# Kernel optimization log

Measured on AMD Instinct MI355X. Metric: run time of the kernel, lower is better.

Reference implementation:

```python
import jax, jax.numpy as jnp
import numpy as np

B, T, I, H = 64, 2048, 256, 256


def setup_inputs() -> dict:
    key = jax.random.key(0)
    ks = jax.random.split(key, 6)
    s = 1.0 / np.sqrt(H)
    x = jax.random.normal(ks[0], (B, T, I), dtype=jnp.float32)
    att_weights = jax.random.uniform(ks[1], (B, T), dtype=jnp.float32)
    lengths = jax.random.randint(ks[2], (B,), 1, T + 1, dtype=jnp.int32)
    W_ih = jax.random.uniform(ks[3], (3 * H, I), minval=-s, maxval=s, dtype=jnp.float32)
    W_hh = jax.random.uniform(ks[4], (3 * H, H), minval=-s, maxval=s, dtype=jnp.float32)
    b_ih = jax.random.uniform(ks[5], (3 * H,), minval=-s, maxval=s, dtype=jnp.float32)
    b_hh = jax.random.uniform(jax.random.fold_in(key, 7), (3 * H,), minval=-s, maxval=s, dtype=jnp.float32)
    return {"x": x, "att_weights": att_weights, "lengths": lengths,
            "W_ih": W_ih, "W_hh": W_hh, "b_ih": b_ih, "b_hh": b_hh}


def reference(x, att_weights, lengths, W_ih, W_hh, b_ih, b_hh):
    # x: [B, T, I]; att_weights: [B, T]; lengths: [B]
    Bv, Tv, _ = x.shape
    Hv = W_hh.shape[1]
    # Padded equivalent of the packed-sequence loop: update h only while t < length.
    mask = jnp.arange(Tv)[None, :] < lengths[:, None]  # [B, T]

    def step(h, inp):
        xt, wt, mt = inp  # [B, I], [B], [B]
        gi = xt @ W_ih.T + b_ih  # [B, 3H]
        gh = h @ W_hh.T + b_hh   # [B, 3H]
        i_r, i_z, i_n = jnp.split(gi, 3, axis=-1)
        h_r, h_z, h_n = jnp.split(gh, 3, axis=-1)
        r = jax.nn.sigmoid(i_r + h_r)
        z = jax.nn.sigmoid(i_z + h_z)
        n = jnp.tanh(i_n + r * h_n)
        h_new = (1.0 - z) * n + z * h  # GRUCell output
        w = wt[:, None]
        h_gated = w * h_new + (1.0 - w) * h  # attention gating
        h = jnp.where(mt[:, None], h_gated, h)
        return h, None

    h0 = jnp.zeros((Bv, Hv), dtype=x.dtype)
    xs = (jnp.swapaxes(x, 0, 1), att_weights.T, mask.T)  # time-major
    hT, _ = jax.lax.scan(step, h0, xs)
    return hT  # [B, H]
```

## Files before the change

kernel.cpp:

```cpp
#include <hip/hip_runtime.h>
#include <stdint.h>

#define B_ 64
#define T_ 2048
#define I_ 256
#define H_ 256
#define G3 768

typedef _Float16 half2v __attribute__((ext_vector_type(2)));
typedef _Float16 half8v __attribute__((ext_vector_type(8)));

#if __has_builtin(__builtin_amdgcn_fdot2)
#define FDOT2(a, b, c) __builtin_amdgcn_fdot2((a), (b), (c), false)
#else
#define FDOT2(a, b, c) fmaf((float)(a)[1], (float)(b)[1], fmaf((float)(a)[0], (float)(b)[0], (c)))
#endif

__global__ __launch_bounds__(256) void gi_gemm(
    const float* __restrict__ x, const float* __restrict__ Wih,
    const float* __restrict__ bih, const float* __restrict__ bhh,
    float* __restrict__ gi, int t0)
{
  const int t  = t0 + blockIdx.x;
  const int n0 = blockIdx.y * 64;
  __shared__ float As[32][68];
  __shared__ float Bs[32][68];
  const int tid = threadIdx.x;
  const int ty = tid >> 4, tx = tid & 15;
  const int lr = tid >> 3;
  const int lk = (tid & 7) << 2;
  float acc[4][4] = {};

  for (int kc = 0; kc < I_; kc += 32) {
    float4 a0 = *(const float4*)(x + ((size_t)lr        * T_ + t) * I_ + kc + lk);
    float4 a1 = *(const float4*)(x + ((size_t)(lr + 32) * T_ + t) * I_ + kc + lk);
    float4 b0 = *(const float4*)(Wih + (size_t)(n0 + lr)      * I_ + kc + lk);
    float4 b1 = *(const float4*)(Wih + (size_t)(n0 + lr + 32) * I_ + kc + lk);
    __syncthreads();
    As[lk+0][lr]    = a0.x; As[lk+1][lr]    = a0.y; As[lk+2][lr]    = a0.z; As[lk+3][lr]    = a0.w;
    As[lk+0][lr+32] = a1.x; As[lk+1][lr+32] = a1.y; As[lk+2][lr+32] = a1.z; As[lk+3][lr+32] = a1.w;
    Bs[lk+0][lr]    = b0.x; Bs[lk+1][lr]    = b0.y; Bs[lk+2][lr]    = b0.z; Bs[lk+3][lr]    = b0.w;
    Bs[lk+0][lr+32] = b1.x; Bs[lk+1][lr+32] = b1.y; Bs[lk+2][lr+32] = b1.z; Bs[lk+3][lr+32] = b1.w;
    __syncthreads();
    #pragma unroll
    for (int kk = 0; kk < 32; ++kk) {
      float4 av = *(const float4*)(&As[kk][ty << 2]);
      float4 bv = *(const float4*)(&Bs[kk][tx << 2]);
      float av_[4] = {av.x, av.y, av.z, av.w};
      float bv_[4] = {bv.x, bv.y, bv.z, bv.w};
      #pragma unroll
      for (int i = 0; i < 4; ++i)
        #pragma unroll
        for (int u = 0; u < 4; ++u)
          acc[i][u] = fmaf(av_[i], bv_[u], acc[i][u]);
    }
  }

  const int colb = n0 + (tx << 2);
  float4 bi = *(const float4*)(bih + colb);
  float4 bh = *(const float4*)(bhh + colb);
  float4 badd;
  badd.x = bi.x + (colb + 0 < 512 ? bh.x : 0.f);
  badd.y = bi.y + (colb + 1 < 512 ? bh.y : 0.f);
  badd.z = bi.z + (colb + 2 < 512 ? bh.z : 0.f);
  badd.w = bi.w + (colb + 3 < 512 ? bh.w : 0.f);
  float* gout = gi + (size_t)blockIdx.x * 64 * G3;
  #pragma unroll
  for (int i = 0; i < 4; ++i) {
    int bb = (ty << 2) + i;
    float4 o;
    o.x = acc[i][0] + badd.x; o.y = acc[i][1] + badd.y;
    o.z = acc[i][2] + badd.z; o.w = acc[i][3] + badd.w;
    *(float4*)(gout + (size_t)bb * G3 + colb) = o;
  }
}

__global__ __launch_bounds__(512) __attribute__((amdgpu_waves_per_eu(2, 2)))
void gru_seq16(const float* __restrict__ gi, const float* __restrict__ att,
               const int* __restrict__ lengths, const float* __restrict__ Whh,
               const float* __restrict__ bhh, float* __restrict__ hws,
               float* __restrict__ out, int t0, int t1)
{
  const int b   = blockIdx.x;
  const int tid = threadIdx.x;
  const int j   = tid >> 1;
  const int s   = tid & 1;
  const int k0  = s << 7;

  __shared__ _Float16 hbuf[2][272];

  half2v w[192];
  #pragma unroll
  for (int g = 0; g < 3; ++g) {
    const float* row = Whh + (size_t)(g * 256 + j) * H_ + k0;
    #pragma unroll
    for (int q = 0; q < 32; ++q) {
      float4 v = *(const float4*)(row + (q << 2));
      half2v a, c;
      a[0] = (_Float16)v.x; a[1] = (_Float16)v.y;
      c[0] = (_Float16)v.z; c[1] = (_Float16)v.w;
      w[g * 64 + 2 * q]     = a;
      w[g * 64 + 2 * q + 1] = c;
    }
  }

  float bhn = 0.f, h_reg = 0.f;
  if (s == 0) {
    bhn = bhh[512 + j];
    h_reg = (t0 > 0) ? hws[b * H_ + j] : 0.f;
  }
  if (tid < 256) {
    float v = (t0 > 0) ? hws[b * H_ + tid] : 0.f;
    hbuf[0][(tid >> 7) * 136 + (tid & 127)] = (_Float16)v;
  }
  int len = lengths[b]; if (len > t1) len = t1;
  __syncthreads();

  float c_gr = 0.f, c_gz = 0.f, c_gn = 0.f, c_wat = 0.f;
  if (s == 0 && t0 < len) {
    const float* gb = gi + (size_t)b * G3;
    c_gr = gb[j]; c_gz = gb[256 + j]; c_gn = gb[512 + j];
    c_wat = att[(size_t)b * T_ + t0];
  }

  int p = 0;
  for (int t = t0; t < len; ++t) {
    float n_gr = 0.f, n_gz = 0.f, n_gn = 0.f, n_wat = 0.f;
    if (s == 0 && t + 1 < len) {
      const float* gb = gi + ((size_t)(t + 1 - t0) * 64 + b) * G3;
      n_gr = gb[j]; n_gz = gb[256 + j]; n_gn = gb[512 + j];
      n_wat = att[(size_t)b * T_ + t + 1];
    }

    float accr = 0.f, accz = 0.f, accn = 0.f;
    const _Float16* hb = &hbuf[p][s * 136];
    #pragma unroll
    for (int q = 0; q < 16; ++q) {
      half8v hv = *(const half8v*)(hb + (q << 3));
      half2v h0 = __builtin_shufflevector(hv, hv, 0, 1);
      half2v h1 = __builtin_shufflevector(hv, hv, 2, 3);
      half2v h2 = __builtin_shufflevector(hv, hv, 4, 5);
      half2v h3 = __builtin_shufflevector(hv, hv, 6, 7);
      const int qq = q << 2;
      accr = FDOT2(w[qq + 0], h0, accr);
      accr = FDOT2(w[qq + 1], h1, accr);
      accr = FDOT2(w[qq + 2], h2, accr);
      accr = FDOT2(w[qq + 3], h3, accr);
      accz = FDOT2(w[64 + qq + 0], h0, accz);
      accz = FDOT2(w[64 + qq + 1], h1, accz);
      accz = FDOT2(w[64 + qq + 2], h2, accz);
      accz = FDOT2(w[64 + qq + 3], h3, accz);
      accn = FDOT2(w[128 + qq + 0], h0, accn);
      accn = FDOT2(w[128 + qq + 1], h1, accn);
      accn = FDOT2(w[128 + qq + 2], h2, accn);
      accn = FDOT2(w[128 + qq + 3], h3, accn);
    }
    accr += __shfl_xor(accr, 1);
    accz += __shfl_xor(accz, 1);
    accn += __shfl_xor(accn, 1);

    if (s == 0) {
      float r = 1.f / (1.f + __expf(-(accr + c_gr)));
      float z = 1.f / (1.f + __expf(-(accz + c_gz)));
      float e2 = __expf(2.f * (c_gn + r * (accn + bhn)));
      float nn = 1.f - 2.f / (e2 + 1.f);
      float hnew = (1.f - z) * nn + z * h_reg;
      h_reg = c_wat * hnew + (1.f - c_wat) * h_reg;
      hbuf[p ^ 1][(j >> 7) * 136 + (j & 127)] = (_Float16)h_reg;
    }
    __syncthreads();
    p ^= 1;
    c_gr = n_gr; c_gz = n_gz; c_gn = n_gn; c_wat = n_wat;
  }

  if (s == 0) {
    hws[b * H_ + j] = h_reg;
    if (t1 == T_) out[b * H_ + j] = h_reg;
  }
}

extern "C" void kernel_launch(void* const* d_in, const int* in_sizes, int n_in,
                              void* d_out, int out_size, void* d_ws, size_t ws_size,
                              hipStream_t stream)
{
  const float* x       = (const float*)d_in[0];
  const float* att     = (const float*)d_in[1];
  const int*   lengths = (const int*)d_in[2];
  const float* Wih     = (const float*)d_in[3];
  const float* Whh     = (const float*)d_in[4];
  const float* bih     = (const float*)d_in[5];
  const float* bhh     = (const float*)d_in[6];
  float* out = (float*)d_out;

  float* hws = (float*)d_ws;
  float* gi  = (float*)((char*)d_ws + 65536);
  const size_t used0 = 65536;
  const size_t per_t = (size_t)B_ * G3 * sizeof(float);
  size_t avail = ws_size > used0 ? ws_size - used0 : 0;
  int Tc = (int)(avail / per_t);
  if (Tc > T_) Tc = T_;
  if (Tc < 1) Tc = 1;

  for (int t0 = 0; t0 < T_; t0 += Tc) {
    int t1 = t0 + Tc; if (t1 > T_) t1 = T_;
    dim3 g1(t1 - t0, G3 / 64);
    gi_gemm<<<g1, 256, 0, stream>>>(x, Wih, bih, bhh, gi, t0);
    gru_seq16<<<B_, 512, 0, stream>>>(gi, att, lengths, Whh, bhh, hws, out, t0, t1);
  }
}
```

Before: 3.421 ms.

## Split GRU recurrent dot product across four lanes per hidden unit

The recurrent kernel now uses 1024 threads per batch block, with four lanes per hidden unit, each holding a quarter of the W_hh rows in registers. This halves per-lane register weights and the serial FDOT2 chain per step, at the cost of an extra shuffle-reduction stage and a barrier spanning twice as many waves. The per-step gate-input loads are also spread across three lanes, with the n-gate value shuffled back to the lane that does the update.

```diff
diff --git a/kernel.cpp b/kernel.cpp
--- a/kernel.cpp
+++ b/kernel.cpp
@@ -75,7 +75,7 @@
   }
 }
 
-__global__ __launch_bounds__(512) __attribute__((amdgpu_waves_per_eu(2, 2)))
+__global__ __launch_bounds__(1024)
 void gru_seq16(const float* __restrict__ gi, const float* __restrict__ att,
                const int* __restrict__ lengths, const float* __restrict__ Whh,
                const float* __restrict__ bhh, float* __restrict__ hws,
@@ -83,24 +83,24 @@
 {
   const int b   = blockIdx.x;
   const int tid = threadIdx.x;
-  const int j   = tid >> 1;
-  const int s   = tid & 1;
-  const int k0  = s << 7;
-
-  __shared__ _Float16 hbuf[2][272];
-
-  half2v w[192];
+  const int j   = tid >> 2;
+  const int s   = tid & 3;
+  const int k0  = s << 6;
+
+  __shared__ _Float16 hbuf[2][288];
+
+  half2v w[96];
   #pragma unroll
   for (int g = 0; g < 3; ++g) {
     const float* row = Whh + (size_t)(g * 256 + j) * H_ + k0;
     #pragma unroll
-    for (int q = 0; q < 32; ++q) {
+    for (int q = 0; q < 16; ++q) {
       float4 v = *(const float4*)(row + (q << 2));
       half2v a, c;
       a[0] = (_Float16)v.x; a[1] = (_Float16)v.y;
       c[0] = (_Float16)v.z; c[1] = (_Float16)v.w;
-      w[g * 64 + 2 * q]     = a;
-      w[g * 64 + 2 * q + 1] = c;
+      w[g * 32 + 2 * q]     = a;
+      w[g * 32 + 2 * q + 1] = c;
     }
   }
 
@@ -111,31 +111,31 @@
   }
   if (tid < 256) {
     float v = (t0 > 0) ? hws[b * H_ + tid] : 0.f;
-    hbuf[0][(tid >> 7) * 136 + (tid & 127)] = (_Float16)v;
+    hbuf[0][(tid >> 6) * 72 + (tid & 63)] = (_Float16)v;
   }
   int len = lengths[b]; if (len > t1) len = t1;
   __syncthreads();
 
-  float c_gr = 0.f, c_gz = 0.f, c_gn = 0.f, c_wat = 0.f;
-  if (s == 0 && t0 < len) {
+  float c_g = 0.f, c_wat = 0.f;
+  if (t0 < len) {
     const float* gb = gi + (size_t)b * G3;
-    c_gr = gb[j]; c_gz = gb[256 + j]; c_gn = gb[512 + j];
-    c_wat = att[(size_t)b * T_ + t0];
+    if (s < 3) c_g = gb[s * 256 + j];
+    if (s == 0) c_wat = att[(size_t)b * T_ + t0];
   }
 
   int p = 0;
   for (int t = t0; t < len; ++t) {
-    float n_gr = 0.f, n_gz = 0.f, n_gn = 0.f, n_wat = 0.f;
-    if (s == 0 && t + 1 < len) {
+    float n_g = 0.f, n_wat = 0.f;
+    if (t + 1 < len) {
       const float* gb = gi + ((size_t)(t + 1 - t0) * 64 + b) * G3;
-      n_gr = gb[j]; n_gz = gb[256 + j]; n_gn = gb[512 + j];
-      n_wat = att[(size_t)b * T_ + t + 1];
+      if (s < 3) n_g = gb[s * 256 + j];
+      if (s == 0) n_wat = att[(size_t)b * T_ + t + 1];
     }
 
     float accr = 0.f, accz = 0.f, accn = 0.f;
-    const _Float16* hb = &hbuf[p][s * 136];
+    const _Float16* hb = &hbuf[p][s * 72];
     #pragma unroll
-    for (int q = 0; q < 16; ++q) {
+    for (int q = 0; q < 8; ++q) {
       half8v hv = *(const half8v*)(hb + (q << 3));
       half2v h0 = __builtin_shufflevector(hv, hv, 0, 1);
       half2v h1 = __builtin_shufflevector(hv, hv, 2, 3);
@@ -146,31 +146,34 @@
       accr = FDOT2(w[qq + 1], h1, accr);
       accr = FDOT2(w[qq + 2], h2, accr);
       accr = FDOT2(w[qq + 3], h3, accr);
-      accz = FDOT2(w[64 + qq + 0], h0, accz);
-      accz = FDOT2(w[64 + qq + 1], h1, accz);
-      accz = FDOT2(w[64 + qq + 2], h2, accz);
-      accz = FDOT2(w[64 + qq + 3], h3, accz);
-      accn = FDOT2(w[128 + qq + 0], h0, accn);
-      accn = FDOT2(w[128 + qq + 1], h1, accn);
-      accn = FDOT2(w[128 + qq + 2], h2, accn);
-      accn = FDOT2(w[128 + qq + 3], h3, accn);
-    }
-    accr += __shfl_xor(accr, 1);
-    accz += __shfl_xor(accz, 1);
-    accn += __shfl_xor(accn, 1);
+      accz = FDOT2(w[32 + qq + 0], h0, accz);
+      accz = FDOT2(w[32 + qq + 1], h1, accz);
+      accz = FDOT2(w[32 + qq + 2], h2, accz);
+      accz = FDOT2(w[32 + qq + 3], h3, accz);
+      accn = FDOT2(w[64 + qq + 0], h0, accn);
+      accn = FDOT2(w[64 + qq + 1], h1, accn);
+      accn = FDOT2(w[64 + qq + 2], h2, accn);
+      accn = FDOT2(w[64 + qq + 3], h3, accn);
+    }
+    if (s == 0)      accr += c_g;
+    else if (s == 1) accz += c_g;
+    accr += __shfl_xor(accr, 1); accr += __shfl_xor(accr, 2);
+    accz += __shfl_xor(accz, 1); accz += __shfl_xor(accz, 2);
+    accn += __shfl_xor(accn, 1); accn += __shfl_xor(accn, 2);
+    float gn = __shfl(c_g, 2, 4);
 
     if (s == 0) {
-      float r = 1.f / (1.f + __expf(-(accr + c_gr)));
-      float z = 1.f / (1.f + __expf(-(accz + c_gz)));
-      float e2 = __expf(2.f * (c_gn + r * (accn + bhn)));
+      float r = 1.f / (1.f + __expf(-accr));
+      float z = 1.f / (1.f + __expf(-accz));
+      float e2 = __expf(2.f * (gn + r * (accn + bhn)));
       float nn = 1.f - 2.f / (e2 + 1.f);
       float hnew = (1.f - z) * nn + z * h_reg;
       h_reg = c_wat * hnew + (1.f - c_wat) * h_reg;
-      hbuf[p ^ 1][(j >> 7) * 136 + (j & 127)] = (_Float16)h_reg;
+      hbuf[p ^ 1][(j >> 6) * 72 + (j & 63)] = (_Float16)h_reg;
     }
     __syncthreads();
     p ^= 1;
-    c_gr = n_gr; c_gz = n_gz; c_gn = n_gn; c_wat = n_wat;
+    c_g = n_g; c_wat = n_wat;
   }
 
   if (s == 0) {
@@ -205,6 +208,6 @@
     int t1 = t0 + Tc; if (t1 > T_) t1 = T_;
     dim3 g1(t1 - t0, G3 / 64);
     gi_gemm<<<g1, 256, 0, stream>>>(x, Wih, bih, bhh, gi, t0);
-    gru_seq16<<<B_, 512, 0, stream>>>(gi, att, lengths, Whh, bhh, hws, out, t0, t1);
+    gru_seq16<<<B_, 1024, 0, stream>>>(gi, att, lengths, Whh, bhh, hws, out, t0, t1);
   }
 }
```

After: 3.913 ms. 14.4% more time.
